# Optimization experiments

Hardware: AMD Instinct MI355X
Metric: run time of the kernel (lower is better)

The kernel has to match this reference:

```python
import jax, jax.numpy as jnp
import numpy as np

S, D, H, HD, CQ, CKV, O = 2048, 2048, 16, 128, 96, 512, 2048


def _linear_params(k, fan_in, fan_out):
    kw, kb = jax.random.split(k)
    lim = 1.0 / np.sqrt(fan_in)
    w = jax.random.uniform(kw, (fan_out, fan_in), minval=-lim, maxval=lim, dtype=jnp.float32)
    b = jax.random.uniform(kb, (fan_out,), minval=-lim, maxval=lim, dtype=jnp.float32)
    return w, b


def setup_inputs() -> dict:
    key = jax.random.key(0)
    ks = jax.random.split(key, 8)
    x = jax.random.normal(ks[0], (S, D), dtype=jnp.float32)
    # standard RoPE tables: theta_i = 10000^(-2i/hd), rotate-half layout
    pos = jnp.arange(S, dtype=jnp.float32)[:, None]              # (S, 1)
    inv_freq = 1.0 / (10000.0 ** (jnp.arange(0, HD, 2, dtype=jnp.float32) / HD))  # (HD/2,)
    ang = pos * inv_freq[None, :]                                 # (S, HD/2)
    rope_cos = jnp.concatenate([jnp.cos(ang), jnp.cos(ang)], axis=-1)  # (S, HD)
    rope_sin = jnp.concatenate([jnp.sin(ang), jnp.sin(ang)], axis=-1)  # (S, HD)
    wq_down, bq_down = _linear_params(ks[1], D, CQ)
    wq_up, bq_up = _linear_params(ks[2], CQ, H * HD)
    wkv_down, bkv_down = _linear_params(ks[3], D, CKV)
    wk_up, bk_up = _linear_params(ks[4], CKV, H * HD)
    wv_up, bv_up = _linear_params(ks[5], CKV, H * HD)
    wo, bo = _linear_params(ks[6], H * HD, O)
    return dict(x=x, rope_cos=rope_cos, rope_sin=rope_sin,
                wq_down=wq_down, bq_down=bq_down, wq_up=wq_up, bq_up=bq_up,
                wkv_down=wkv_down, bkv_down=bkv_down, wk_up=wk_up, bk_up=bk_up,
                wv_up=wv_up, bv_up=bv_up, wo=wo, bo=bo)


def _rope(xh, cos, sin):
    # xh: (S, H, hd); cos/sin: (S, hd) broadcast over heads
    half = xh.shape[-1] // 2
    x1, x2 = xh[..., :half], xh[..., half:]
    rot = jnp.concatenate([-x2, x1], axis=-1)
    return xh * cos[:, None, :] + rot * sin[:, None, :]


def reference(x, rope_cos, rope_sin, wq_down, bq_down, wq_up, bq_up,
              wkv_down, bkv_down, wk_up, bk_up, wv_up, bv_up, wo, bo):
    s = x.shape[0]
    # low-rank Q path: down then up (compressed_q_size < head_dim branch)
    c_q = x @ wq_down.T + bq_down                                  # (S, CQ)
    q = (c_q @ wq_up.T + bq_up).reshape(s, H, HD)                  # (S, H, hd)
    q = _rope(q, rope_cos, rope_sin)
    # shared compressed KV path
    c_kv = x @ wkv_down.T + bkv_down                               # (S, CKV)
    k = _rope((c_kv @ wk_up.T + bk_up).reshape(s, H, HD), rope_cos, rope_sin)
    v = (c_kv @ wv_up.T + bv_up).reshape(s, H, HD)
    # scaled dot-product attention per head (softmax in fp32 as in source)
    q = q / jnp.sqrt(jnp.asarray(HD, q.dtype))
    logits = jnp.einsum('shd,Shd->hsS', q, k)                      # (H, S, S)
    weights = jax.nn.softmax(logits.astype(jnp.float32), axis=-1).astype(logits.dtype)
    attn = jnp.einsum('hsS,Shd->shd', weights, v).reshape(s, H * HD)
    return attn @ wo.T + bo                                        # (S, O)
```

## Files before the change

### kernel.cpp

```cpp
#include <hip/hip_runtime.h>
#include <cstdint>
#include <cstddef>

typedef unsigned short u16;
typedef float f32x4 __attribute__((ext_vector_type(4)));
typedef short s16x8 __attribute__((ext_vector_type(8)));

#define DI __device__ __forceinline__

static constexpr int S_  = 2048;
static constexpr int D_  = 2048;
static constexpr int H_  = 16;
static constexpr int HD_ = 128;
static constexpr int HHD = 2048;
static constexpr int CQP = 128;
static constexpr int NCAT = 640;
static constexpr int CKV_ = 512;
static constexpr float QSCALE = 0.12751743360294163f;

DI u16 f2bf(float f) {
  unsigned u = __float_as_uint(f);
  u += 0x7fffu + ((u >> 16) & 1u);
  return (u16)(u >> 16);
}
DI float bf2f(u16 h) { return __uint_as_float(((unsigned)h) << 16); }

DI void store_c(float* C, long long i, float v) { C[i] = v; }
DI void store_c(u16* C, long long i, float v) { C[i] = f2bf(v); }

template <int CTRL>
DI float dppf(float x) {
  return __uint_as_float((unsigned)__builtin_amdgcn_mov_dpp(
      (int)__float_as_uint(x), CTRL, 0xf, 0xf, true));
}
DI float red_max16(float x) {
  x = fmaxf(x, dppf<0xB1>(x));
  x = fmaxf(x, dppf<0x4E>(x));
  x = fmaxf(x, dppf<0x141>(x));
  x = fmaxf(x, dppf<0x140>(x));
  return x;
}
DI float red_sum16(float x) {
  x += dppf<0xB1>(x);
  x += dppf<0x4E>(x);
  x += dppf<0x141>(x);
  x += dppf<0x140>(x);
  return x;
}

#define GLD16(g, l)                                                        \
  __builtin_amdgcn_global_load_lds(                                        \
      (__attribute__((address_space(1))) void*)(void*)(const void*)(g),    \
      (__attribute__((address_space(3))) void*)(l), 16, 0, 0)

template <typename OutT, int BCOL, int BROW, int ROPE, int BN>
DI void gemm_core(u16* __restrict__ Asm, u16* __restrict__ Bsm,
                  const u16* __restrict__ A, const u16* __restrict__ B,
                  OutT* __restrict__ C,
                  const float* __restrict__ bias_col,
                  const float* __restrict__ bias_row,
                  int K, int lda, int ldb, int ldc,
                  const float* __restrict__ rcs, const float* __restrict__ rsn,
                  float scale) {
  constexpr int MI = (BN == 128) ? 4 : 2;
  constexpr int NI = 4;
  constexpr int NCH = 8 + BN / 16;
  constexpr int NC4 = NCH / 4;
  const int tid  = threadIdx.x;
  const int w    = tid >> 6;
  const int lane = tid & 63;
  const int lr   = lane & 15;
  const int lq   = lane >> 4;
  const long long m0 = (long long)blockIdx.y * 128;
  const long long n0 = (long long)blockIdx.x * BN;
  const int wr = (BN == 128) ? (w >> 1) * 64 : w * 32;
  const int wc = (BN == 128) ? (w & 1) * 64 : 0;

  f32x4 acc[MI][NI];
#pragma unroll
  for (int i = 0; i < MI; ++i)
#pragma unroll
    for (int j = 0; j < NI; ++j)
#pragma unroll
      for (int r = 0; r < 4; ++r) acc[i][j][r] = 0.f;

  const int rch = lane >> 2, cch = (lane & 3) * 8;
  const u16* gsrc[NC4];
  u16* ldst[NC4];
  int bstep[NC4];
#pragma unroll
  for (int ci = 0; ci < NC4; ++ci) {
    const int c = w + ci * 4;
    if (c < 8) {
      gsrc[ci] = A + (m0 + c * 16 + rch) * lda + cch;
      ldst[ci] = &Asm[c * 512];
      bstep[ci] = 128 * 32;
    } else {
      gsrc[ci] = B + (n0 + (c - 8) * 16 + rch) * ldb + cch;
      ldst[ci] = &Bsm[(c - 8) * 512];
      bstep[ci] = BN * 32;
    }
  }
  auto stage = [&](int kt, int b) {
#pragma unroll
    for (int ci = 0; ci < NC4; ++ci) GLD16(gsrc[ci] + kt, ldst[ci] + b * bstep[ci]);
  };

  stage(0, 0);
  int cur = 0;
  for (int kt = 0; kt < K; kt += 32) {
    __syncthreads();
    if (kt + 32 < K) stage(kt + 32, cur ^ 1);
    const u16* Ab = &Asm[cur * 128 * 32];
    const u16* Bb = &Bsm[cur * BN * 32];

    s16x8 af[MI], bfr[NI];
#pragma unroll
    for (int tm = 0; tm < MI; ++tm)
      af[tm] = *(const s16x8*)&Ab[(wr + tm * 16 + lr) * 32 + lq * 8];
#pragma unroll
    for (int tn = 0; tn < NI; ++tn) {
      const int cb = ROPE ? ((w & 1) * 32 + (tn & 1) * 16 + (tn >> 1) * 64)
                          : (wc + tn * 16);
      bfr[tn] = *(const s16x8*)&Bb[(cb + lr) * 32 + lq * 8];
    }
#pragma unroll
    for (int tm = 0; tm < MI; ++tm)
#pragma unroll
      for (int tn = 0; tn < NI; ++tn)
        acc[tm][tn] = __builtin_amdgcn_mfma_f32_16x16x32_bf16(af[tm], bfr[tn],
                                                              acc[tm][tn], 0, 0, 0);
    cur ^= 1;
  }

  if (ROPE) {
#pragma unroll
    for (int tm = 0; tm < MI; ++tm)
#pragma unroll
      for (int tn = 0; tn < 2; ++tn) {
        const long long col1 = n0 + (w & 1) * 32 + tn * 16 + lr;
        const long long col2 = col1 + 64;
        const float bc1 = bias_col[col1];
        const float bc2 = bias_col[col2];
        const int dd = (int)(col1 & 127);
#pragma unroll
        for (int r = 0; r < 4; ++r) {
          const long long row = m0 + wr + tm * 16 + lq * 4 + r;
          const float c = rcs[row * 128 + dd];
          const float s = rsn[row * 128 + dd];
          const float v1 = acc[tm][tn][r] + bc1;
          const float v2 = acc[tm][tn + 2][r] + bc2;
          store_c(C, row * (long long)ldc + col1, (v1 * c - v2 * s) * scale);
          store_c(C, row * (long long)ldc + col2, (v2 * c + v1 * s) * scale);
        }
      }
  } else {
#pragma unroll
    for (int tm = 0; tm < MI; ++tm)
#pragma unroll
      for (int tn = 0; tn < NI; ++tn) {
        const long long col = n0 + wc + tn * 16 + lr;
        float bc = BCOL ? bias_col[col] : 0.f;
#pragma unroll
        for (int r = 0; r < 4; ++r) {
          const long long row = m0 + wr + tm * 16 + lq * 4 + r;
          float v = acc[tm][tn][r] + bc;
          if (BROW) v += bias_row[row];
          store_c(C, row * (long long)ldc + col, v);
        }
      }
  }
}

template <typename OutT, int BCOL, int BROW, int BN>
__global__ __launch_bounds__(256) void gemm_bt(
    const u16* __restrict__ A, const u16* __restrict__ B, OutT* __restrict__ C,
    const float* __restrict__ bias_col, const float* __restrict__ bias_row,
    int K, int lda, int ldb, int ldc,
    long long sA, long long sB, long long sC) {
  __shared__ __align__(16) u16 As[2 * 128 * 32];
  __shared__ __align__(16) u16 Bs[2 * BN * 32];
  gemm_core<OutT, BCOL, BROW, 0, BN>(
      As, Bs, A + (long long)blockIdx.z * sA, B + (long long)blockIdx.z * sB,
      C + (long long)blockIdx.z * sC, bias_col, bias_row, K, lda, ldb, ldc,
      nullptr, nullptr, 0.f);
}

__global__ __launch_bounds__(256, 3) void up3(
    const u16* __restrict__ ccat, const u16* __restrict__ wqu,
    const u16* __restrict__ wku, const u16* __restrict__ wvu,
    const float* __restrict__ bq_up, const float* __restrict__ bk_up,
    const float* __restrict__ bv_up,
    const float* __restrict__ rcs, const float* __restrict__ rsn,
    u16* __restrict__ qb, u16* __restrict__ kb, u16* __restrict__ vT) {
  __shared__ __align__(16) u16 As[2 * 128 * 32];
  __shared__ __align__(16) u16 Bs[2 * 128 * 32];
  if (blockIdx.z == 0)
    gemm_core<u16, 1, 0, 1, 128>(As, Bs, ccat, wqu, qb, bq_up, nullptr,
                                 CQP, NCAT, CQP, HHD, rcs, rsn, QSCALE);
  else if (blockIdx.z == 1)
    gemm_core<u16, 1, 0, 1, 128>(As, Bs, ccat + CQP, wku, kb, bk_up, nullptr,
                                 CKV_, NCAT, CKV_, HHD, rcs, rsn, 1.0f);
  else
    gemm_core<u16, 0, 1, 0, 128>(As, Bs, wvu, ccat + CQP, vT, nullptr, bv_up,
                                 CKV_, CKV_, NCAT, S_, nullptr, nullptr, 0.f);
}

DI void store4(float* d, long long e, float4 s) { *(float4*)(d + e) = s; }
DI void store4(u16* d, long long e, float4 s) {
  unsigned lo = (unsigned)f2bf(s.x) | ((unsigned)f2bf(s.y) << 16);
  unsigned hi = (unsigned)f2bf(s.z) | ((unsigned)f2bf(s.w) << 16);
  *(uint2*)(d + e) = make_uint2(lo, hi);
}
template <typename OutT>
__global__ __launch_bounds__(256) void combine_z(
    const float* __restrict__ p, long long zs, int nz,
    const float* __restrict__ bias, OutT* __restrict__ dst, int ldc, int n4) {
  int i = blockIdx.x * 256 + threadIdx.x;
  if (i >= n4) return;
  long long e = (long long)i * 4;
  float4 s = *(const float4*)(p + e);
  for (int z = 1; z < nz; ++z) {
    float4 t = *(const float4*)(p + (long long)z * zs + e);
    s.x += t.x; s.y += t.y; s.z += t.z; s.w += t.w;
  }
  int c = (int)(e % ldc);
  s.x += bias[c]; s.y += bias[c + 1]; s.z += bias[c + 2]; s.w += bias[c + 3];
  store4(dst, e, s);
}

__global__ __launch_bounds__(256, 2) void flash_attn(
    const u16* __restrict__ Q, const u16* __restrict__ Kg,
    const u16* __restrict__ Vt, u16* __restrict__ Og) {
  __shared__ __align__(16) u16 Ks[128 * 128];
  __shared__ __align__(16) u16 Vs[128 * 128];
  __shared__ __align__(16) u16 Ps[64 * 128];
  const int h = blockIdx.x;
  const int t = blockIdx.y;
  const int tid = threadIdx.x;
  const int w = tid >> 6, lane = tid & 63, lr = lane & 15, lq = lane >> 4;
  const int g = w >> 1;
  const int wq = w & 1;
  const int qw = t * 64 + wq * 32;
  const int tr = tid >> 4;
  const int csw = (tid & 15) ^ (tr & 7);

  s16x8 qf[2][4];
#pragma unroll
  for (int mi = 0; mi < 2; ++mi)
#pragma unroll
    for (int kst = 0; kst < 4; ++kst)
      qf[mi][kst] = *(const s16x8*)&Q[(size_t)(qw + mi * 16 + lr) * HHD +
                                      h * HD_ + kst * 32 + lq * 8];

  f32x4 oacc[2][8];
  float m[2][4], l[2][4];
#pragma unroll
  for (int mi = 0; mi < 2; ++mi) {
#pragma unroll
    for (int r = 0; r < 4; ++r) { m[mi][r] = -1.0e38f; l[mi][r] = 0.f; }
#pragma unroll
    for (int f = 0; f < 8; ++f)
#pragma unroll
      for (int r = 0; r < 4; ++r) oacc[mi][f][r] = 0.f;
  }

  auto stage_k = [&](int j) {
    const u16* s0 = Kg + (size_t)(j * 128 + tr) * HHD + h * HD_ + csw * 8;
#pragma unroll
    for (int i = 0; i < 8; ++i)
      GLD16(s0 + (size_t)i * 16 * HHD, &Ks[i * 2048 + w * 512]);
  };
  auto stage_v = [&](int j) {
    const u16* s0 = Vt + (size_t)(h * HD_ + tr) * S_ + j * 128 + csw * 8;
#pragma unroll
    for (int i = 0; i < 8; ++i)
      GLD16(s0 + (size_t)i * 16 * S_, &Vs[i * 2048 + w * 512]);
  };

  stage_k(0);
  stage_v(0);
  __syncthreads();

  for (int j = 0; j < 16; ++j) {
    f32x4 sacc[2][4];
#pragma unroll
    for (int mi = 0; mi < 2; ++mi)
#pragma unroll
      for (int f = 0; f < 4; ++f)
#pragma unroll
        for (int r = 0; r < 4; ++r) sacc[mi][f][r] = 0.f;
#pragma unroll
    for (int kst = 0; kst < 4; ++kst)
#pragma unroll
      for (int f = 0; f < 4; ++f) {
        const int key = g * 64 + f * 16 + lr;
        s16x8 kf = *(const s16x8*)
            &Ks[key * 128 + (((kst * 4 + lq) ^ (key & 7)) << 3)];
        sacc[0][f] = __builtin_amdgcn_mfma_f32_16x16x32_bf16(qf[0][kst], kf,
                                                             sacc[0][f], 0, 0, 0);
        sacc[1][f] = __builtin_amdgcn_mfma_f32_16x16x32_bf16(qf[1][kst], kf,
                                                             sacc[1][f], 0, 0, 0);
      }

#pragma unroll
    for (int mi = 0; mi < 2; ++mi) {
      float mx[4];
      bool need = false;
#pragma unroll
      for (int r = 0; r < 4; ++r) {
        float v = sacc[mi][0][r];
#pragma unroll
        for (int f = 1; f < 4; ++f) v = fmaxf(v, sacc[mi][f][r]);
        mx[r] = red_max16(v);
        need = need || (mx[r] > m[mi][r]);
      }
      if (__any(need)) {
#pragma unroll
        for (int r = 0; r < 4; ++r) {
          float mn = fmaxf(m[mi][r], mx[r]);
          float al = exp2f(m[mi][r] - mn);
          m[mi][r] = mn;
          l[mi][r] *= al;
#pragma unroll
          for (int f = 0; f < 8; ++f) oacc[mi][f][r] *= al;
        }
      }
#pragma unroll
      for (int r = 0; r < 4; ++r) {
        float sum = 0.f;
#pragma unroll
        for (int f = 0; f < 4; ++f) {
          float p = exp2f(sacc[mi][f][r] - m[mi][r]);
          sacc[mi][f][r] = p;
          sum += p;
        }
        l[mi][r] += sum;
      }
    }

#pragma unroll
    for (int mi = 0; mi < 2; ++mi)
#pragma unroll
      for (int r = 0; r < 4; ++r) {
        const int q = wq * 32 + mi * 16 + lq * 4 + r;
#pragma unroll
        for (int f = 0; f < 4; ++f) {
          const int ch = (g * 8 + f * 2 + (lr >> 3)) ^ (q & 7);
          Ps[q * 128 + ch * 8 + (lr & 7)] = f2bf(sacc[mi][f][r]);
        }
      }

    __syncthreads();
    if (j < 15) stage_k(j + 1);

#pragma unroll
    for (int kst = 0; kst < 2; ++kst) {
      const int chA = (g * 8 + kst * 4 + lq) ^ (lr & 7);
      s16x8 pa0 = *(const s16x8*)&Ps[(wq * 32 + lr) * 128 + chA * 8];
      s16x8 pa1 = *(const s16x8*)&Ps[(wq * 32 + 16 + lr) * 128 + chA * 8];
#pragma unroll
      for (int f = 0; f < 8; ++f) {
        const int d = f * 16 + lr;
        s16x8 vf = *(const s16x8*)
            &Vs[d * 128 + (((g * 8 + kst * 4 + lq) ^ (d & 7)) << 3)];
        oacc[0][f] = __builtin_amdgcn_mfma_f32_16x16x32_bf16(pa0, vf,
                                                             oacc[0][f], 0, 0, 0);
        oacc[1][f] = __builtin_amdgcn_mfma_f32_16x16x32_bf16(pa1, vf,
                                                             oacc[1][f], 0, 0, 0);
      }
    }

    __syncthreads();
    if (j < 15) stage_v(j + 1);
  }

  float lf[2][4];
#pragma unroll
  for (int mi = 0; mi < 2; ++mi)
#pragma unroll
    for (int r = 0; r < 4; ++r) lf[mi][r] = red_sum16(l[mi][r]);

  float* KsF = (float*)Ks;
  float* mlF = (float*)Ps;
  if (g == 1) {
#pragma unroll
    for (int mi = 0; mi < 2; ++mi)
#pragma unroll
      for (int r = 0; r < 4; ++r) {
        const int q = wq * 32 + mi * 16 + lq * 4 + r;
        if (lr == 0) { mlF[q * 2] = m[mi][r]; mlF[q * 2 + 1] = lf[mi][r]; }
#pragma unroll
        for (int f = 0; f < 8; ++f)
          KsF[q * 128 + f * 16 + lr] = oacc[mi][f][r];
      }
  }
  __syncthreads();
  if (g == 0) {
#pragma unroll
    for (int mi = 0; mi < 2; ++mi)
#pragma unroll
      for (int r = 0; r < 4; ++r) {
        const int q = wq * 32 + mi * 16 + lq * 4 + r;
        float m1 = mlF[q * 2], l1 = mlF[q * 2 + 1];
        float M = fmaxf(m[mi][r], m1);
        float w0 = exp2f(m[mi][r] - M), w1 = exp2f(m1 - M);
        float inv = 1.f / (w0 * lf[mi][r] + w1 * l1);
        w0 *= inv; w1 *= inv;
#pragma unroll
        for (int f = 0; f < 8; ++f) {
          float o = w0 * oacc[mi][f][r] + w1 * KsF[q * 128 + f * 16 + lr];
          Og[(size_t)(t * 64 + q) * HHD + h * HD_ + f * 16 + lr] = f2bf(o);
        }
      }
  }
}

DI void cast4(const float* __restrict__ s, u16* __restrict__ d, int v) {
  float4 f = ((const float4*)s)[v];
  unsigned lo = (unsigned)f2bf(f.x) | ((unsigned)f2bf(f.y) << 16);
  unsigned hi = (unsigned)f2bf(f.z) | ((unsigned)f2bf(f.w) << 16);
  ((uint2*)d)[v] = make_uint2(lo, hi);
}
DI void store_bf4(u16* __restrict__ d, long long i, float4 f) {
  unsigned lo = (unsigned)f2bf(f.x) | ((unsigned)f2bf(f.y) << 16);
  unsigned hi = (unsigned)f2bf(f.z) | ((unsigned)f2bf(f.w) << 16);
  *(uint2*)(d + i) = make_uint2(lo, hi);
}
static constexpr int PV_XB   = 1048576;
static constexpr int PV_WCAT = 327680;
static constexpr int PV_WQU  = 65536;
static constexpr int PV_WKU  = 262144;
static constexpr int PV_WVU  = 262144;
static constexpr int PV_WOB  = 1048576;
static constexpr int PV_BCAT = 160;
static constexpr int PV_TOT  = PV_XB + PV_WCAT + PV_WQU + PV_WKU + PV_WVU + PV_WOB + PV_BCAT;

__global__ __launch_bounds__(256) void prep(
    const float* __restrict__ x, const float* __restrict__ wqd_s,
    const float* __restrict__ wkvd_s, const float* __restrict__ wqu_s,
    const float* __restrict__ wku_s, const float* __restrict__ wvu_s,
    const float* __restrict__ wo_s, const float* __restrict__ bqd_s,
    const float* __restrict__ bkvd_s,
    u16* __restrict__ xb, u16* __restrict__ wcat, u16* __restrict__ wqu,
    u16* __restrict__ wku, u16* __restrict__ wvu, u16* __restrict__ wob,
    float* __restrict__ bcat) {
  int v = blockIdx.x * 256 + threadIdx.x;
  if (v >= PV_TOT) return;
  if (v < PV_XB) { cast4(x, xb, v); return; }
  v -= PV_XB;
  if (v < PV_WCAT) {
    int i = v * 4, n = i >> 11, k = i & 2047;
    float4 o = make_float4(0.f, 0.f, 0.f, 0.f);
    if (n < 96)        o = *(const float4*)&wqd_s[n * D_ + k];
    else if (n >= 128) o = *(const float4*)&wkvd_s[(n - 128) * D_ + k];
    store_bf4(wcat, i, o);
    return;
  }
  v -= PV_WCAT;
  if (v < PV_WQU) {
    int i = v * 4, r = i >> 7, c = i & 127;
    float4 o = (c < 96) ? *(const float4*)&wqu_s[r * 96 + c]
                        : make_float4(0.f, 0.f, 0.f, 0.f);
    store_bf4(wqu, i, o);
    return;
  }
  v -= PV_WQU;
  if (v < PV_WKU) { cast4(wku_s, wku, v); return; }
  v -= PV_WKU;
  if (v < PV_WVU) { cast4(wvu_s, wvu, v); return; }
  v -= PV_WVU;
  if (v < PV_WOB) { cast4(wo_s, wob, v); return; }
  v -= PV_WOB;
  {
    int i = v * 4;
    float4 o;
    float* po = &o.x;
#pragma unroll
    for (int jj = 0; jj < 4; ++jj) {
      int e = i + jj;
      po[jj] = (e < 96) ? bqd_s[e] : (e < 128 ? 0.f : bkvd_s[e - 128]);
    }
    *(float4*)&bcat[i] = o;
  }
}

extern "C" void kernel_launch(void* const* d_in, const int* in_sizes, int n_in,
                              void* d_out, int out_size, void* d_ws, size_t ws_size,
                              hipStream_t stream) {
  (void)in_sizes; (void)n_in; (void)out_size; (void)ws_size;
  const float* x        = (const float*)d_in[0];
  const float* rc       = (const float*)d_in[1];
  const float* rs       = (const float*)d_in[2];
  const float* wq_down  = (const float*)d_in[3];
  const float* bq_down  = (const float*)d_in[4];
  const float* wq_up    = (const float*)d_in[5];
  const float* bq_up    = (const float*)d_in[6];
  const float* wkv_down = (const float*)d_in[7];
  const float* bkv_down = (const float*)d_in[8];
  const float* wk_up    = (const float*)d_in[9];
  const float* bk_up    = (const float*)d_in[10];
  const float* wv_up    = (const float*)d_in[11];
  const float* bv_up    = (const float*)d_in[12];
  const float* wo       = (const float*)d_in[13];
  const float* bo       = (const float*)d_in[14];
  float* out = (float*)d_out;

  char* ws = (char*)d_ws;
  size_t off = 0;
  auto alloc = [&](size_t bytes) -> void* {
    off = (off + 255) & ~(size_t)255;
    void* p = ws + off;
    off += bytes;
    return p;
  };

  u16* xb      = (u16*)alloc((size_t)S_ * D_ * 2);
  u16* wcat    = (u16*)alloc((size_t)NCAT * D_ * 2);
  float* bcat  = (float*)alloc(NCAT * 4);
  u16* wqu     = (u16*)alloc((size_t)HHD * CQP * 2);
  u16* wku     = (u16*)alloc((size_t)HHD * CKV_ * 2);
  u16* wvu     = (u16*)alloc((size_t)HHD * CKV_ * 2);
  u16* wob     = (u16*)alloc((size_t)D_ * HHD * 2);
  u16* ccat    = (u16*)alloc((size_t)S_ * NCAT * 2);
  u16* qb      = (u16*)alloc((size_t)S_ * HHD * 2);
  u16* kb      = (u16*)alloc((size_t)S_ * HHD * 2);
  u16* vT      = (u16*)alloc((size_t)HHD * S_ * 2);
  u16* attnb   = (u16*)alloc((size_t)S_ * HHD * 2);
  float* pool  = (float*)alloc((size_t)2 * S_ * D_ * 4);
  float* pcat  = pool;
  float* pout  = pool;

  prep<<<(PV_TOT + 255) / 256, 256, 0, stream>>>(
      x, wq_down, wkv_down, wq_up, wk_up, wv_up, wo, bq_down, bkv_down,
      xb, wcat, wqu, wku, wvu, wob, bcat);

  gemm_bt<float, 0, 0, 64><<<dim3(NCAT / 64, 16, 4), 256, 0, stream>>>(
      xb, wcat, pcat, nullptr, nullptr, 512, D_, D_, NCAT,
      512, 512, (long long)S_ * NCAT);
  combine_z<u16><<<(S_ * NCAT / 4 + 255) / 256, 256, 0, stream>>>(
      pcat, (long long)S_ * NCAT, 4, bcat, ccat, NCAT, S_ * NCAT / 4);

  up3<<<dim3(16, 16, 3), 256, 0, stream>>>(
      ccat, wqu, wku, wvu, bq_up, bk_up, bv_up, rc, rs, qb, kb, vT);

  flash_attn<<<dim3(H_, S_ / 64, 1), 256, 0, stream>>>(qb, kb, vT, attnb);

  gemm_bt<float, 0, 0, 128><<<dim3(16, 16, 2), 256, 0, stream>>>(
      attnb, wob, pout, nullptr, nullptr, 1024, HHD, HHD, D_,
      1024, 1024, (long long)S_ * D_);
  combine_z<float><<<(S_ * D_ / 4 + 255) / 256, 256, 0, stream>>>(
      pout, (long long)S_ * D_, 2, bo, out, D_, S_ * D_ / 4);
}
```

Before: 268.5 us.

## Fuse split-K reduction into GEMM via last-block atomic counter

Replaces the split-K GEMM plus separate combine kernel with one kernel. Each z-slice writes its fp32 partial tile, and the last block to finish a tile, found through an atomic counter, sums all slices, adds the bias and writes the output. This removes two extra kernel launches and the separate pass that reread the partials. The output projection also moves from split-K 2 to split-K 4 for more parallelism, at the cost of a larger partial buffer, more partial traffic and counters that prep must zero.

```diff
diff --git a/kernel.cpp b/kernel.cpp
--- a/kernel.cpp
+++ b/kernel.cpp
@@ -172,20 +172,6 @@
   }
 }
 
-template <typename OutT, int BCOL, int BROW, int BN>
-__global__ __launch_bounds__(256) void gemm_bt(
-    const u16* __restrict__ A, const u16* __restrict__ B, OutT* __restrict__ C,
-    const float* __restrict__ bias_col, const float* __restrict__ bias_row,
-    int K, int lda, int ldb, int ldc,
-    long long sA, long long sB, long long sC) {
-  __shared__ __align__(16) u16 As[2 * 128 * 32];
-  __shared__ __align__(16) u16 Bs[2 * BN * 32];
-  gemm_core<OutT, BCOL, BROW, 0, BN>(
-      As, Bs, A + (long long)blockIdx.z * sA, B + (long long)blockIdx.z * sB,
-      C + (long long)blockIdx.z * sC, bias_col, bias_row, K, lda, ldb, ldc,
-      nullptr, nullptr, 0.f);
-}
-
 __global__ __launch_bounds__(256, 3) void up3(
     const u16* __restrict__ ccat, const u16* __restrict__ wqu,
     const u16* __restrict__ wku, const u16* __restrict__ wvu,
@@ -212,21 +198,126 @@
   unsigned hi = (unsigned)f2bf(s.z) | ((unsigned)f2bf(s.w) << 16);
   *(uint2*)(d + e) = make_uint2(lo, hi);
 }
-template <typename OutT>
-__global__ __launch_bounds__(256) void combine_z(
-    const float* __restrict__ p, long long zs, int nz,
-    const float* __restrict__ bias, OutT* __restrict__ dst, int ldc, int n4) {
-  int i = blockIdx.x * 256 + threadIdx.x;
-  if (i >= n4) return;
-  long long e = (long long)i * 4;
-  float4 s = *(const float4*)(p + e);
-  for (int z = 1; z < nz; ++z) {
-    float4 t = *(const float4*)(p + (long long)z * zs + e);
-    s.x += t.x; s.y += t.y; s.z += t.z; s.w += t.w;
-  }
-  int c = (int)(e % ldc);
-  s.x += bias[c]; s.y += bias[c + 1]; s.z += bias[c + 2]; s.w += bias[c + 3];
-  store4(dst, e, s);
+
+template <typename OutT, int BN, int NZ>
+__global__ __launch_bounds__(256) void gemm_red(
+    const u16* __restrict__ A, const u16* __restrict__ B,
+    float* __restrict__ pbuf, OutT* __restrict__ C,
+    const float* __restrict__ bias_col, int* __restrict__ cnt,
+    int Kz, int lda, int ldb, int ldc) {
+  constexpr int MI = (BN == 128) ? 4 : 2;
+  constexpr int NI = 4;
+  constexpr int NCH = 8 + BN / 16;
+  constexpr int NC4 = NCH / 4;
+  __shared__ __align__(16) u16 As[2 * 128 * 32];
+  __shared__ __align__(16) u16 Bs[2 * BN * 32];
+  const int tid  = threadIdx.x;
+  const int w    = tid >> 6;
+  const int lane = tid & 63;
+  const int lr   = lane & 15;
+  const int lq   = lane >> 4;
+  const long long m0 = (long long)blockIdx.y * 128;
+  const long long n0 = (long long)blockIdx.x * BN;
+  const int wr = (BN == 128) ? (w >> 1) * 64 : w * 32;
+  const int wc = (BN == 128) ? (w & 1) * 64 : 0;
+  const int z = blockIdx.z;
+  A += (long long)z * Kz;
+  B += (long long)z * Kz;
+
+  f32x4 acc[MI][NI];
+#pragma unroll
+  for (int i = 0; i < MI; ++i)
+#pragma unroll
+    for (int j = 0; j < NI; ++j)
+#pragma unroll
+      for (int r = 0; r < 4; ++r) acc[i][j][r] = 0.f;
+
+  const int rch = lane >> 2, cch = (lane & 3) * 8;
+  const u16* gsrc[NC4];
+  u16* ldst[NC4];
+  int bstep[NC4];
+#pragma unroll
+  for (int ci = 0; ci < NC4; ++ci) {
+    const int c = w + ci * 4;
+    if (c < 8) {
+      gsrc[ci] = A + (m0 + c * 16 + rch) * lda + cch;
+      ldst[ci] = &As[c * 512];
+      bstep[ci] = 128 * 32;
+    } else {
+      gsrc[ci] = B + (n0 + (c - 8) * 16 + rch) * ldb + cch;
+      ldst[ci] = &Bs[(c - 8) * 512];
+      bstep[ci] = BN * 32;
+    }
+  }
+  auto stage = [&](int kt, int b) {
+#pragma unroll
+    for (int ci = 0; ci < NC4; ++ci) GLD16(gsrc[ci] + kt, ldst[ci] + b * bstep[ci]);
+  };
+
+  stage(0, 0);
+  int cur = 0;
+  for (int kt = 0; kt < Kz; kt += 32) {
+    __syncthreads();
+    if (kt + 32 < Kz) stage(kt + 32, cur ^ 1);
+    const u16* Ab = &As[cur * 128 * 32];
+    const u16* Bb = &Bs[cur * BN * 32];
+
+    s16x8 af[MI], bfr[NI];
+#pragma unroll
+    for (int tm = 0; tm < MI; ++tm)
+      af[tm] = *(const s16x8*)&Ab[(wr + tm * 16 + lr) * 32 + lq * 8];
+#pragma unroll
+    for (int tn = 0; tn < NI; ++tn)
+      bfr[tn] = *(const s16x8*)&Bb[(wc + tn * 16 + lr) * 32 + lq * 8];
+#pragma unroll
+    for (int tm = 0; tm < MI; ++tm)
+#pragma unroll
+      for (int tn = 0; tn < NI; ++tn)
+        acc[tm][tn] = __builtin_amdgcn_mfma_f32_16x16x32_bf16(af[tm], bfr[tn],
+                                                              acc[tm][tn], 0, 0, 0);
+    cur ^= 1;
+  }
+
+  const long long MN = (long long)gridDim.y * 128 * ldc;
+  float* pp = pbuf + (long long)z * MN;
+#pragma unroll
+  for (int tm = 0; tm < MI; ++tm)
+#pragma unroll
+    for (int tn = 0; tn < NI; ++tn) {
+      const long long col = n0 + wc + tn * 16 + lr;
+#pragma unroll
+      for (int r = 0; r < 4; ++r) {
+        const long long row = m0 + wr + tm * 16 + lq * 4 + r;
+        pp[row * (long long)ldc + col] = acc[tm][tn][r];
+      }
+    }
+
+  __threadfence();
+  __shared__ int lastf;
+  if (tid == 0)
+    lastf = (atomicAdd(&cnt[blockIdx.y * gridDim.x + blockIdx.x], 1) == NZ - 1);
+  __syncthreads();
+  if (!lastf) return;
+  __threadfence();
+
+  constexpr int ITER = 128 * BN / 4 / 256;
+  const long long base = m0 * (long long)ldc + n0;
+  for (int it = 0; it < ITER; ++it) {
+    const int e4 = it * 256 + tid;
+    const int r = e4 / (BN / 4);
+    const int c = (e4 % (BN / 4)) * 4;
+    const long long gi = base + (long long)r * ldc + c;
+    float4 s = *(const float4*)&pbuf[gi];
+#pragma unroll
+    for (int zz = 1; zz < NZ; ++zz) {
+      float4 t = *(const float4*)&pbuf[(long long)zz * MN + gi];
+      s.x += t.x; s.y += t.y; s.z += t.z; s.w += t.w;
+    }
+    const int bc = (int)(n0 + c);
+    s.x += bias_col[bc]; s.y += bias_col[bc + 1];
+    s.z += bias_col[bc + 2]; s.w += bias_col[bc + 3];
+    store4(C, gi, s);
+  }
 }
 
 __global__ __launch_bounds__(256, 2) void flash_attn(
@@ -434,7 +525,9 @@
 static constexpr int PV_WVU  = 262144;
 static constexpr int PV_WOB  = 1048576;
 static constexpr int PV_BCAT = 160;
-static constexpr int PV_TOT  = PV_XB + PV_WCAT + PV_WQU + PV_WKU + PV_WVU + PV_WOB + PV_BCAT;
+static constexpr int PV_CNT  = 128;
+static constexpr int PV_TOT  = PV_XB + PV_WCAT + PV_WQU + PV_WKU + PV_WVU +
+                               PV_WOB + PV_BCAT + PV_CNT;
 
 __global__ __launch_bounds__(256) void prep(
     const float* __restrict__ x, const float* __restrict__ wqd_s,
@@ -444,7 +537,7 @@
     const float* __restrict__ bkvd_s,
     u16* __restrict__ xb, u16* __restrict__ wcat, u16* __restrict__ wqu,
     u16* __restrict__ wku, u16* __restrict__ wvu, u16* __restrict__ wob,
-    float* __restrict__ bcat) {
+    float* __restrict__ bcat, int* __restrict__ cnt) {
   int v = blockIdx.x * 256 + threadIdx.x;
   if (v >= PV_TOT) return;
   if (v < PV_XB) { cast4(x, xb, v); return; }
@@ -472,7 +565,7 @@
   v -= PV_WVU;
   if (v < PV_WOB) { cast4(wo_s, wob, v); return; }
   v -= PV_WOB;
-  {
+  if (v < PV_BCAT) {
     int i = v * 4;
     float4 o;
     float* po = &o.x;
@@ -482,7 +575,10 @@
       po[jj] = (e < 96) ? bqd_s[e] : (e < 128 ? 0.f : bkvd_s[e - 128]);
     }
     *(float4*)&bcat[i] = o;
-  }
+    return;
+  }
+  v -= PV_BCAT;
+  ((uint4*)cnt)[v] = make_uint4(0, 0, 0, 0);
 }
 
 extern "C" void kernel_launch(void* const* d_in, const int* in_sizes, int n_in,
@@ -527,28 +623,25 @@
   u16* kb      = (u16*)alloc((size_t)S_ * HHD * 2);
   u16* vT      = (u16*)alloc((size_t)HHD * S_ * 2);
   u16* attnb   = (u16*)alloc((size_t)S_ * HHD * 2);
-  float* pool  = (float*)alloc((size_t)2 * S_ * D_ * 4);
+  int* cnt     = (int*)alloc(512 * 4);
+  float* pool  = (float*)alloc((size_t)4 * S_ * D_ * 4);
   float* pcat  = pool;
   float* pout  = pool;
+  int* cnt_c   = cnt;
+  int* cnt_o   = cnt + 160;
 
   prep<<<(PV_TOT + 255) / 256, 256, 0, stream>>>(
       x, wq_down, wkv_down, wq_up, wk_up, wv_up, wo, bq_down, bkv_down,
-      xb, wcat, wqu, wku, wvu, wob, bcat);
-
-  gemm_bt<float, 0, 0, 64><<<dim3(NCAT / 64, 16, 4), 256, 0, stream>>>(
-      xb, wcat, pcat, nullptr, nullptr, 512, D_, D_, NCAT,
-      512, 512, (long long)S_ * NCAT);
-  combine_z<u16><<<(S_ * NCAT / 4 + 255) / 256, 256, 0, stream>>>(
-      pcat, (long long)S_ * NCAT, 4, bcat, ccat, NCAT, S_ * NCAT / 4);
+      xb, wcat, wqu, wku, wvu, wob, bcat, cnt);
+
+  gemm_red<u16, 64, 4><<<dim3(NCAT / 64, 16, 4), 256, 0, stream>>>(
+      xb, wcat, pcat, ccat, bcat, cnt_c, 512, D_, D_, NCAT);
 
   up3<<<dim3(16, 16, 3), 256, 0, stream>>>(
       ccat, wqu, wku, wvu, bq_up, bk_up, bv_up, rc, rs, qb, kb, vT);
 
   flash_attn<<<dim3(H_, S_ / 64, 1), 256, 0, stream>>>(qb, kb, vT, attnb);
 
-  gemm_bt<float, 0, 0, 128><<<dim3(16, 16, 2), 256, 0, stream>>>(
-      attnb, wob, pout, nullptr, nullptr, 1024, HHD, HHD, D_,
-      1024, 1024, (long long)S_ * D_);
-  combine_z<float><<<(S_ * D_ / 4 + 255) / 256, 256, 0, stream>>>(
-      pout, (long long)S_ * D_, 2, bo, out, D_, S_ * D_ / 4);
-}
+  gemm_red<float, 128, 4><<<dim3(16, 16, 4), 256, 0, stream>>>(
+      attnb, wob, pout, out, bo, cnt_o, 512, HHD, HHD, D_);
+}
```

Measured after the change: 555.6 us. 107% more time.
